# Kernel tuning notes

Hardware: AMD Instinct MI355X
Metric: run time of the kernel (lower is better)

## Reference

```python
import jax, jax.numpy as jnp
import numpy as np

B, T, D, H, L = 16, 1024, 1024, 1024, 2


def setup_inputs() -> dict:
    key = jax.random.key(0)
    ks = jax.random.split(key, 7)
    s_ih = float(np.sqrt(6.0 / (4 * H + D)))  # xavier_uniform bound
    s_hh = float(np.sqrt(6.0 / (4 * H + H)))
    return {
        "x": jax.random.normal(ks[0], (B, T, D), dtype=jnp.float32),
        "w_ih0": jax.random.uniform(ks[1], (4 * H, D), jnp.float32, -s_ih, s_ih),
        "w_hh0": jax.random.uniform(ks[2], (4 * H, H), jnp.float32, -s_hh, s_hh),
        "b0": jnp.zeros((4 * H,), jnp.float32),
        "w_ih1": jax.random.uniform(ks[3], (4 * H, H), jnp.float32, -s_ih, s_ih),
        "w_hh1": jax.random.uniform(ks[4], (4 * H, H), jnp.float32, -s_hh, s_hh),
        "b1": jnp.zeros((4 * H,), jnp.float32),
    }


def _cell(x, h, c, w_ih, w_hh, b):
    # gates: [B, 4H]
    gates = x @ w_ih.T + h @ w_hh.T + b
    i, f, g, o = jnp.split(gates, 4, axis=1)
    i = jnp.exp(i)            # exponential input gate (xLSTM sLSTM)
    f = jnp.exp(f)            # exponential forget gate
    g = jnp.tanh(g)
    o = jax.nn.sigmoid(o)
    c = f * c + i * g
    h = o * jnp.tanh(c)
    return h, c


def reference(x, w_ih0, w_hh0, b0, w_ih1, w_hh1, b1):
    b = x.shape[0]
    zeros = jnp.zeros((b, H), x.dtype)
    init = (zeros, zeros, zeros, zeros)  # (h0, c0, h1, c1)

    def step(carry, xt):
        h0, c0, h1, c1 = carry
        h0, c0 = _cell(xt, h0, c0, w_ih0, w_hh0, b0)
        h1, c1 = _cell(h0, h1, c1, w_ih1, w_hh1, b1)
        return (h0, c0, h1, c1), h1

    carry, ys = jax.lax.scan(step, init, jnp.swapaxes(x, 0, 1))  # time-major scan
    out = jnp.swapaxes(ys, 0, 1)  # [B, T, H]
    h0, c0, h1, c1 = carry
    return out, h0, c0, h1, c1
```

## Files before the change

kernel.cpp:

```cpp
#include <hip/hip_runtime.h>
#include <math.h>

namespace {
constexpr int Bt   = 16;
constexpr int Tt   = 1024;
constexpr int Hd   = 1024;
constexpr int NT   = 512;
constexpr int UPB  = 8;
constexpr int NROW = 32;
constexpr int BH   = Bt * Hd;

typedef unsigned long long u64;

__device__ __forceinline__ float sanitize_c(float v) {
  return fminf(fmaxf(v, -3.0e38f), 3.0e38f);
}

template <int CTRL>
__device__ __forceinline__ float dpp_add(float v) {
  int x = __builtin_amdgcn_update_dpp(0, __float_as_int(v), CTRL, 0xF, 0xF, true);
  return v + __int_as_float(x);
}
__device__ __forceinline__ float red8(float v) {
  v = dpp_add<0xB1>(v);
  v = dpp_add<0x4E>(v);
  v = dpp_add<0x141>(v);
  return v;
}

__device__ __forceinline__ void st_h32(float* p, float v) {
  __hip_atomic_store(p, v, __ATOMIC_RELAXED, __HIP_MEMORY_SCOPE_AGENT);
}

#define LD16(d, p) asm volatile("global_load_dwordx4 %0, %1, off sc1" \
                                : "=v"(d) : "v"(p) : "memory")
#define STAGE_SLAB(dst, src, sIdx) { \
  _Pragma("unroll") \
  for (int q = 0; q < 2; ++q) { \
    float4 t0,t1,t2,t3,t4,t5,t6,t7; \
    const int base_ = q * 8192 + (sIdx) * 4; \
    LD16(t0, (src) + base_);        LD16(t1, (src) + base_ + 1024); \
    LD16(t2, (src) + base_ + 2048); LD16(t3, (src) + base_ + 3072); \
    LD16(t4, (src) + base_ + 4096); LD16(t5, (src) + base_ + 5120); \
    LD16(t6, (src) + base_ + 6144); LD16(t7, (src) + base_ + 7168); \
    asm volatile("s_waitcnt vmcnt(0)" ::: "memory"); \
    __builtin_amdgcn_sched_barrier(0); \
    *(float4*)((dst) + base_)        = t0; *(float4*)((dst) + base_ + 1024) = t1; \
    *(float4*)((dst) + base_ + 2048) = t2; *(float4*)((dst) + base_ + 3072) = t3; \
    *(float4*)((dst) + base_ + 4096) = t4; *(float4*)((dst) + base_ + 5120) = t5; \
    *(float4*)((dst) + base_ + 6144) = t6; *(float4*)((dst) + base_ + 7168) = t7; \
  } }
}

__global__ __launch_bounds__(NT)
__attribute__((amdgpu_waves_per_eu(2, 2)))
void slstm_persist(
    const float* __restrict__ x,
    const float* __restrict__ wih0, const float* __restrict__ whh0, const float* __restrict__ b0v,
    const float* __restrict__ wih1, const float* __restrict__ whh1, const float* __restrict__ b1v,
    float* __restrict__ out, float* __restrict__ ws)
{
  __shared__ __align__(16) float in0[BH];
  __shared__ __align__(16) float in1[BH];
  __shared__ __align__(16) float red[64 * 17 * 4];
  __shared__ float gatel[NROW * Bt];
  __shared__ float cst[UPB * Bt];
  __shared__ float biasl[NROW];

  const int tid  = threadIdx.x;
  const int bid  = blockIdx.x;
  const int w    = tid >> 6;
  const int lane = tid & 63;
  const int kslo = lane & 7;
  const int rg   = lane >> 3;
  const int ks   = w * 8 + kslo;
  const bool isB = ks >= 32;
  const int ksl  = ks & 31;
  const int cell = bid >> 7;
  const int blk  = bid & 127;
  const int ubase = blk * UPB;

  unsigned* flags = (unsigned*)ws;
  float* h0buf = ws + 1024;
  float* h1buf = h0buf + 3 * BH;

  const float* wmat = (cell == 0) ? (isB ? whh0 : wih0) : (isB ? whh1 : wih1);
  const float* bv   = (cell == 0) ? b0v : b1v;

  const int ro0 = ((0 + kslo) & 7) * 16;
  const int ro1 = ((1 + kslo) & 7) * 16;
  const int ro2 = ((2 + kslo) & 7) * 16;
  const int ro3 = ((3 + kslo) & 7) * 16;
  const int ro4 = ((4 + kslo) & 7) * 16;
  const int ro5 = ((5 + kslo) & 7) * 16;
  const int ro6 = ((6 + kslo) & 7) * 16;
  const int ro7 = ((7 + kslo) & 7) * 16;

  float4 w00,w01,w02,w03,w04,w05,w06,w07;
  float4 w10,w11,w12,w13,w14,w15,w16,w17;
  float4 w20,w21,w22,w23,w24,w25,w26,w27;
  float4 w30,w31,w32,w33,w34,w35,w36,w37;
#define LDW(r) { \
    const int lr = rg * 4 + r; \
    const char* wb = (const char*)(wmat + (size_t)((lr >> 3) * Hd + ubase + (lr & 7)) * Hd + ksl * 32); \
    w##r##0 = *(const float4*)(wb + ro0); w##r##1 = *(const float4*)(wb + ro1); \
    w##r##2 = *(const float4*)(wb + ro2); w##r##3 = *(const float4*)(wb + ro3); \
    w##r##4 = *(const float4*)(wb + ro4); w##r##5 = *(const float4*)(wb + ro5); \
    w##r##6 = *(const float4*)(wb + ro6); w##r##7 = *(const float4*)(wb + ro7); }
  LDW(0) LDW(1) LDW(2) LDW(3)
#undef LDW

  if (tid < NROW) biasl[tid] = bv[(tid >> 3) * Hd + ubase + (tid & 7)];
  if (tid < UPB * Bt) cst[tid] = 0.f;

  if (cell == 0) {
    #pragma unroll
    for (int p = 0; p < 8; ++p) {
      const int e = p * 2048 + tid * 4;
      const int b = e >> 10, d = e & 1023;
      *(float4*)(in0 + e) = *(const float4*)(x + (size_t)b * (Tt * Hd) + d);
    }
  }
  __syncthreads();

#define STEPC(c) { const float4 v = *(const float4*)(pb + ro##c); \
        a0 = fmaf(v.x, w0##c.x, a0); a0 = fmaf(v.y, w0##c.y, a0); \
        a0 = fmaf(v.z, w0##c.z, a0); a0 = fmaf(v.w, w0##c.w, a0); \
        a1 = fmaf(v.x, w1##c.x, a1); a1 = fmaf(v.y, w1##c.y, a1); \
        a1 = fmaf(v.z, w1##c.z, a1); a1 = fmaf(v.w, w1##c.w, a1); \
        a2 = fmaf(v.x, w2##c.x, a2); a2 = fmaf(v.y, w2##c.y, a2); \
        a2 = fmaf(v.z, w2##c.z, a2); a2 = fmaf(v.w, w2##c.w, a2); \
        a3 = fmaf(v.x, w3##c.x, a3); a3 = fmaf(v.y, w3##c.y, a3); \
        a3 = fmaf(v.z, w3##c.z, a3); a3 = fmaf(v.w, w3##c.w, a3); }
#define MATMUL(INBUF) { \
    const float* myin = (INBUF) + ksl * 32; \
    _Pragma("unroll 2") \
    for (int b = 0; b < Bt; ++b) { \
      const char* pb = (const char*)(myin + b * Hd); \
      float a0 = 0.f, a1 = 0.f, a2 = 0.f, a3 = 0.f; \
      STEPC(0) STEPC(1) STEPC(2) STEPC(3) \
      STEPC(4) STEPC(5) STEPC(6) STEPC(7) \
      a0 = red8(a0); a1 = red8(a1); a2 = red8(a2); a3 = red8(a3); \
      if (kslo == 0) \
        *(float4*)&red[((w * 8 + rg) * 17 + b) * 4] = make_float4(a0, a1, a2, a3); \
    } }

  for (int k = 0; k <= Tt + 1; ++k) {
    const bool act = (cell == 0) ? (k < Tt) : (k >= 2);
    const int s0 = (k + 2) % 3;
    const int s1 = (k + 1) & 1;

    if (w < 4) {
      if (act) { MATMUL(in0) }
    } else {
      const unsigned tgt = (unsigned)k;
      const int f = tid - 256;
      while (__hip_atomic_load(&flags[f], __ATOMIC_RELAXED, __HIP_MEMORY_SCOPE_AGENT) < tgt)
        __builtin_amdgcn_s_sleep(1);
    }
    __syncthreads();

    if (w >= 4) {
      if (act) {
        const int s = tid - 256;
        if ((cell == 0 && k == 0) || (cell == 1 && k == 2)) {
          #pragma unroll
          for (int p = 0; p < 16; ++p)
            *(float4*)(in1 + p * 1024 + s * 4) = make_float4(0.f, 0.f, 0.f, 0.f);
        } else {
          const float* src = (cell == 0) ? (h0buf + s0 * BH) : (h1buf + s1 * BH);
          STAGE_SLAB(in1, src, s)
        }
      }
    } else {
      if (cell == 0) {
        if (k + 1 < Tt) {
          #pragma unroll
          for (int p = 0; p < 16; ++p) {
            const int e = p * 1024 + tid * 4;
            const int b = e >> 10, d = e & 1023;
            *(float4*)(in0 + e) =
                *(const float4*)(x + (size_t)b * (Tt * Hd) + (size_t)(k + 1) * Hd + d);
          }
        }
      } else if (k >= 1 && k <= Tt) {
        const float* src = h0buf + s0 * BH;
        STAGE_SLAB(in0, src, tid)
      }
    }
    __syncthreads();

    float oh = 0.f, oc = 0.f;
    if (act) {
      if (w >= 4) { MATMUL(in1) }
      __syncthreads();

      {
        const int rg2 = tid >> 6, rem = tid & 63, b2 = rem >> 2, r2 = rem & 3;
        float sgm = 0.f;
        #pragma unroll
        for (int ww = 0; ww < 8; ++ww)
          sgm += red[((ww * 8 + rg2) * 17 + b2) * 4 + r2];
        const int lr = rg2 * 4 + r2;
        gatel[lr * Bt + b2] = sgm + biasl[lr];
      }
      __syncthreads();

      if (tid < UPB * Bt) {
        const int u = tid >> 4, b2 = tid & 15;
        const float gi = gatel[(0 * UPB + u) * Bt + b2];
        const float gf = gatel[(1 * UPB + u) * Bt + b2];
        const float gg = gatel[(2 * UPB + u) * Bt + b2];
        const float go = gatel[(3 * UPB + u) * Bt + b2];
        const float ig = expf(gi);
        const float fg = expf(gf);
        const float g_ = tanhf(gg);
        const float og = 1.f / (1.f + expf(-go));
        const float cn = fg * cst[tid] + ig * g_;
        cst[tid] = cn;
        const float h = og * tanhf(cn);
        oh = h; oc = cn;
        const int j = ubase + u;
        if (cell == 0) {
          st_h32(&h0buf[(k % 3) * BH + b2 * Hd + j], h);
        } else {
          st_h32(&h1buf[(k & 1) * BH + b2 * Hd + j], h);
        }
      }
    }

    asm volatile("s_waitcnt vmcnt(0)" ::: "memory");
    __syncthreads();
    if (tid == 0)
      __hip_atomic_store(&flags[bid], (unsigned)(k + 1), __ATOMIC_RELAXED, __HIP_MEMORY_SCOPE_AGENT);

    if (act && tid < UPB * Bt) {
      const int u = tid >> 4, b2 = tid & 15, j = ubase + u;
      const size_t fin = (size_t)Bt * Tt * Hd;
      if (cell == 0) {
        if (k == Tt - 1) {
          out[fin + b2 * Hd + j] = oh;
          out[fin + Bt * Hd + b2 * Hd + j] = sanitize_c(oc);
        }
      } else {
        const int t = k - 2;
        out[((size_t)b2 * Tt + t) * Hd + j] = oh;
        if (t == Tt - 1) {
          out[fin + 2 * Bt * Hd + b2 * Hd + j] = oh;
          out[fin + 3 * Bt * Hd + b2 * Hd + j] = sanitize_c(oc);
        }
      }
    }
  }
  asm volatile("s_waitcnt vmcnt(0)" ::: "memory");
#undef MATMUL
#undef STEPC
}

extern "C" void kernel_launch(void* const* d_in, const int* in_sizes, int n_in,
                              void* d_out, int out_size, void* d_ws, size_t ws_size,
                              hipStream_t stream) {
  (void)hipMemsetAsync(d_ws, 0, 4096, stream);

  const float* x    = (const float*)d_in[0];
  const float* wih0 = (const float*)d_in[1];
  const float* whh0 = (const float*)d_in[2];
  const float* b0   = (const float*)d_in[3];
  const float* wih1 = (const float*)d_in[4];
  const float* whh1 = (const float*)d_in[5];
  const float* b1   = (const float*)d_in[6];

  slstm_persist<<<256, NT, 0, stream>>>(x, wih0, whh0, b0, wih1, whh1, b1,
                                        (float*)d_out, (float*)d_ws);
}
```

Before: 16.85 ms.

## Use block-contiguous hidden-state exchange layout and single-wave vectorized flag polling

Hidden-state buffers are now written in a block-major layout: each block stores its 8 units × 16 batch values as one contiguous 128-float chunk instead of scattered per-batch strided stores. The staging loads gather from that layout back into the batch-major LDS arrays. Flag polling is moved from 256 threads each spinning on one flag to a single wave reading four flags per lane with dwordx4 loads and a wave-wide __all. The goal is to cut cross-block synchronization traffic and make the h-vector stores coalesced. The cost is more scattered gather loads during staging and a different cst indexing order.

New measurement: 17.58 ms. 1.04x slower.

```diff
diff --git a/kernel.cpp b/kernel.cpp
--- a/kernel.cpp
+++ b/kernel.cpp
@@ -34,21 +34,27 @@
 
 #define LD16(d, p) asm volatile("global_load_dwordx4 %0, %1, off sc1" \
                                 : "=v"(d) : "v"(p) : "memory")
-#define STAGE_SLAB(dst, src, sIdx) { \
+
+#define STAGE_GATHER(dst, src, sIdx) { \
+  const int s4_ = (sIdx) * 4; \
+  const float* sb_ = (src) + ((s4_ >> 3) * 128 + (s4_ & 7)); \
   _Pragma("unroll") \
   for (int q = 0; q < 2; ++q) { \
     float4 t0,t1,t2,t3,t4,t5,t6,t7; \
-    const int base_ = q * 8192 + (sIdx) * 4; \
-    LD16(t0, (src) + base_);        LD16(t1, (src) + base_ + 1024); \
-    LD16(t2, (src) + base_ + 2048); LD16(t3, (src) + base_ + 3072); \
-    LD16(t4, (src) + base_ + 4096); LD16(t5, (src) + base_ + 5120); \
-    LD16(t6, (src) + base_ + 6144); LD16(t7, (src) + base_ + 7168); \
+    LD16(t0, sb_ + (q*8+0)*8); LD16(t1, sb_ + (q*8+1)*8); \
+    LD16(t2, sb_ + (q*8+2)*8); LD16(t3, sb_ + (q*8+3)*8); \
+    LD16(t4, sb_ + (q*8+4)*8); LD16(t5, sb_ + (q*8+5)*8); \
+    LD16(t6, sb_ + (q*8+6)*8); LD16(t7, sb_ + (q*8+7)*8); \
     asm volatile("s_waitcnt vmcnt(0)" ::: "memory"); \
     __builtin_amdgcn_sched_barrier(0); \
-    *(float4*)((dst) + base_)        = t0; *(float4*)((dst) + base_ + 1024) = t1; \
-    *(float4*)((dst) + base_ + 2048) = t2; *(float4*)((dst) + base_ + 3072) = t3; \
-    *(float4*)((dst) + base_ + 4096) = t4; *(float4*)((dst) + base_ + 5120) = t5; \
-    *(float4*)((dst) + base_ + 6144) = t6; *(float4*)((dst) + base_ + 7168) = t7; \
+    *(float4*)((dst) + (q*8+0)*1024 + s4_) = t0; \
+    *(float4*)((dst) + (q*8+1)*1024 + s4_) = t1; \
+    *(float4*)((dst) + (q*8+2)*1024 + s4_) = t2; \
+    *(float4*)((dst) + (q*8+3)*1024 + s4_) = t3; \
+    *(float4*)((dst) + (q*8+4)*1024 + s4_) = t4; \
+    *(float4*)((dst) + (q*8+5)*1024 + s4_) = t5; \
+    *(float4*)((dst) + (q*8+6)*1024 + s4_) = t6; \
+    *(float4*)((dst) + (q*8+7)*1024 + s4_) = t7; \
   } }
 }
 
@@ -152,11 +158,17 @@
 
     if (w < 4) {
       if (act) { MATMUL(in0) }
-    } else {
-      const unsigned tgt = (unsigned)k;
-      const int f = tid - 256;
-      while (__hip_atomic_load(&flags[f], __ATOMIC_RELAXED, __HIP_MEMORY_SCOPE_AGENT) < tgt)
+    } else if (w == 4) {
+      const int tgt = k;
+      const unsigned* fp = flags + lane * 4;
+      for (;;) {
+        int4 fv;
+        asm volatile("global_load_dwordx4 %0, %1, off sc1\n\ts_waitcnt vmcnt(0)"
+                     : "=v"(fv) : "v"(fp) : "memory");
+        const bool ok = (fv.x >= tgt) & (fv.y >= tgt) & (fv.z >= tgt) & (fv.w >= tgt);
+        if (__all(ok)) break;
         __builtin_amdgcn_s_sleep(1);
+      }
     }
     __syncthreads();
 
@@ -169,7 +181,7 @@
             *(float4*)(in1 + p * 1024 + s * 4) = make_float4(0.f, 0.f, 0.f, 0.f);
         } else {
           const float* src = (cell == 0) ? (h0buf + s0 * BH) : (h1buf + s1 * BH);
-          STAGE_SLAB(in1, src, s)
+          STAGE_GATHER(in1, src, s)
         }
       }
     } else {
@@ -185,7 +197,7 @@
         }
       } else if (k >= 1 && k <= Tt) {
         const float* src = h0buf + s0 * BH;
-        STAGE_SLAB(in0, src, tid)
+        STAGE_GATHER(in0, src, tid)
       }
     }
     __syncthreads();
@@ -206,8 +218,8 @@
       }
       __syncthreads();
 
-      if (tid < UPB * Bt) {
-        const int u = tid >> 4, b2 = tid & 15;
+      if (tid < 128) {
+        const int u = tid & 7, b2 = (tid >> 3) & 15;
         const float gi = gatel[(0 * UPB + u) * Bt + b2];
         const float gf = gatel[(1 * UPB + u) * Bt + b2];
         const float gg = gatel[(2 * UPB + u) * Bt + b2];
@@ -220,11 +232,10 @@
         cst[tid] = cn;
         const float h = og * tanhf(cn);
         oh = h; oc = cn;
-        const int j = ubase + u;
         if (cell == 0) {
-          st_h32(&h0buf[(k % 3) * BH + b2 * Hd + j], h);
+          st_h32(&h0buf[(k % 3) * BH + blk * 128 + tid], h);
         } else {
-          st_h32(&h1buf[(k & 1) * BH + b2 * Hd + j], h);
+          st_h32(&h1buf[(k & 1) * BH + blk * 128 + tid], h);
         }
       }
     }
@@ -234,8 +245,8 @@
     if (tid == 0)
       __hip_atomic_store(&flags[bid], (unsigned)(k + 1), __ATOMIC_RELAXED, __HIP_MEMORY_SCOPE_AGENT);
 
-    if (act && tid < UPB * Bt) {
-      const int u = tid >> 4, b2 = tid & 15, j = ubase + u;
+    if (act && tid < 128) {
+      const int u = tid & 7, b2 = (tid >> 3) & 15, j = ubase + u;
       const size_t fin = (size_t)Bt * Tt * Hd;
       if (cell == 0) {
         if (k == Tt - 1) {
```
